# Kernel tuning notes

Measured on AMD Instinct MI355X. Metric: run time of the kernel, lower is better.

The kernel has to match this reference:

```python
import jax, jax.numpy as jnp
import numpy as np

B, LC, LT, D = 32, 2048, 512, 256  # D = 2*hidden_dim (bidirectional LSTM output)


def setup_inputs() -> dict:
    key = jax.random.key(0)
    k1, k2 = jax.random.split(key)
    return {
        "context_hidden": jax.random.normal(k1, (B, LC, D), dtype=jnp.float32),
        "target_hidden": jax.random.normal(k2, (B, LT, D), dtype=jnp.float32),
    }


def reference(context_hidden, target_hidden):
    # Pairwise Euclidean distance via |c|^2 + |t|^2 - 2 c.t (replaces the
    # original Python double for-loop of per-pair torch.norm calls).
    c2 = jnp.sum(context_hidden * context_hidden, axis=-1, keepdims=True)      # [B,Lc,1]
    t2 = jnp.sum(target_hidden * target_hidden, axis=-1)[:, None, :]           # [B,1,Lt]
    ct = jnp.einsum('bcd,btd->bct', context_hidden, target_hidden)             # [B,Lc,Lt]
    dist = jnp.sqrt(jnp.maximum(c2 + t2 - 2.0 * ct, 0.0))
    weights = 1.0 / (1.0 + dist)  # G2CT: [B,Lc,Lt]
    # G2C_m = weights @ target ; G2T_m = weights^T @ context (as in forward)
    g2c_m = jnp.einsum('bct,btd->bcd', weights, target_hidden)                 # [B,Lc,D]
    g2t_m = jnp.einsum('bct,bcd->btd', weights, context_hidden)                # [B,Lt,D]
    # concat along sequence axis so the block has a single output tensor
    return jnp.concatenate([g2c_m, g2t_m], axis=1)                             # [B,Lc+Lt,D]
```

## Files before the change

kernel.cpp:

```cpp
#include <hip/hip_runtime.h>

typedef float f32x4 __attribute__((ext_vector_type(4)));
typedef short s16x8 __attribute__((ext_vector_type(8)));

#define NB_    32
#define NLC    2048
#define NLT    512
#define ND     256
#define NCHUNK 512
#define NITER  (NCHUNK / 32)

__device__ __forceinline__ unsigned short f2bf(float f) {
    union { float f; unsigned int u; } v; v.f = f;
    unsigned int r = v.u + 0x7FFFu + ((v.u >> 16) & 1u);
    return (unsigned short)(r >> 16);
}

__device__ __forceinline__ s16x8 cvt8(float4 a, float4 c, float s) {
    s16x8 f;
    f[0]=(short)f2bf(s*a.x); f[1]=(short)f2bf(s*a.y); f[2]=(short)f2bf(s*a.z); f[3]=(short)f2bf(s*a.w);
    f[4]=(short)f2bf(s*c.x); f[5]=(short)f2bf(s*c.y); f[6]=(short)f2bf(s*c.z); f[7]=(short)f2bf(s*c.w);
    return f;
}

__device__ __forceinline__ void glds16(const void* g, void* l) {
    __builtin_amdgcn_global_load_lds(
        (const __attribute__((address_space(1))) unsigned int*)g,
        (__attribute__((address_space(3))) unsigned int*)l, 16, 0, 0);
}

__global__ __launch_bounds__(256) void prep_kernel(
    const float* __restrict__ ctx, const float* __restrict__ tgt,
    float* __restrict__ norms,
    unsigned short* __restrict__ ctxb, unsigned short* __restrict__ tgtb)
{
    const int wave = threadIdx.x >> 6;
    const int lane = threadIdx.x & 63;
    const int rid = blockIdx.x * 4 + wave;
    const float* row;
    unsigned short* drow;
    if (rid < NB_ * NLC) { row = ctx + (size_t)rid * ND; drow = ctxb + (size_t)rid * ND; }
    else { row = tgt + (size_t)(rid - NB_ * NLC) * ND; drow = tgtb + (size_t)(rid - NB_ * NLC) * ND; }
    const float4 v = *(const float4*)(row + lane * 4);
    *(ushort4*)(drow + lane * 4) = make_ushort4(f2bf(v.x), f2bf(v.y), f2bf(v.z), f2bf(v.w));
    float s = v.x * v.x + v.y * v.y + v.z * v.z + v.w * v.w;
    #pragma unroll
    for (int off = 32; off >= 1; off >>= 1) s += __shfl_xor(s, off);
    if (lane == 0) norms[rid] = s;
}

__global__ __launch_bounds__(256) void transpose_bf(
    const unsigned short* __restrict__ ctxb, const unsigned short* __restrict__ tgtb,
    unsigned short* __restrict__ ctxT, unsigned short* __restrict__ tgtT)
{
    __shared__ unsigned short tile[64][72];
    const int id = blockIdx.x;
    const unsigned short* in;
    unsigned short* outp;
    int ldL;
    if (id < 4096) {
        const int b = id >> 7, r = id & 127, lt = r >> 2, dt = r & 3;
        in   = ctxb + ((size_t)b * NLC + lt * 64) * ND + dt * 64;
        outp = ctxT + ((size_t)b * ND + dt * 64) * NLC + lt * 64;
        ldL = NLC;
    } else {
        const int id2 = id - 4096;
        const int b = id2 >> 5, r = id2 & 31, lt = r >> 2, dt = r & 3;
        in   = tgtb + ((size_t)b * NLT + lt * 64) * ND + dt * 64;
        outp = tgtT + ((size_t)b * ND + dt * 64) * NLT + lt * 64;
        ldL = NLT;
    }
    const int t = threadIdx.x;
    const int r0 = t >> 2, c0 = t & 3;
    const s16x8 v0 = *(const s16x8*)&in[(size_t)r0 * ND + c0 * 8];
    const s16x8 v1 = *(const s16x8*)&in[(size_t)r0 * ND + (c0 + 4) * 8];
    *(s16x8*)&tile[r0][c0 * 8] = v0;
    *(s16x8*)&tile[r0][(c0 + 4) * 8] = v1;
    __syncthreads();
    unsigned short buf[16];
    #pragma unroll
    for (int i = 0; i < 16; ++i) buf[i] = tile[(t & 3) * 16 + i][t >> 2];
    unsigned short* op = outp + (size_t)(t >> 2) * ldL + (t & 3) * 16;
    *(s16x8*)&op[0] = *(const s16x8*)&buf[0];
    *(s16x8*)&op[8] = *(const s16x8*)&buf[8];
}

__global__ __launch_bounds__(256, 2) void k1_weights(
    const unsigned short* __restrict__ ctxb, const unsigned short* __restrict__ tgtb,
    const float* __restrict__ norms,
    unsigned short* __restrict__ Wg, unsigned short* __restrict__ WTg)
{
    __shared__ __align__(16) unsigned short Alds[2][128 * 64];
    __shared__ __align__(16) unsigned short Blds[2][128 * 64];
    __shared__ __align__(16) unsigned short relay[4][16 * 128];

    const int phys = blockIdx.x;
    const int L = (phys & 7) * 256 + (phys >> 3);
    const int b = L >> 6;
    const int r = L & 63;
    const int cb = r >> 2, tb = r & 3;

    const int tid = threadIdx.x, wave = tid >> 6, lane = tid & 63;
    const int lr = lane & 15, lq = lane >> 4;
    const int cw = cb * 128 + wave * 32;

    const unsigned short* Actx = ctxb + ((size_t)b * NLC + cb * 128) * ND;
    const unsigned short* Btgt = tgtb + ((size_t)b * NLT + tb * 128) * ND;

    auto STAGE = [&](int buf, int ks) {
        #pragma unroll
        for (int i = 0; i < 4; ++i) {
            const int q = wave * 4 + i;
            const int rloc = q * 8 + (lane >> 3);
            const int gcol = (lane & 7) ^ (rloc & 7);
            glds16(Actx + (size_t)rloc * ND + ks * 64 + gcol * 8, &Alds[buf][q * 512]);
            glds16(Btgt + (size_t)rloc * ND + ks * 64 + gcol * 8, &Blds[buf][q * 512]);
        }
    };

    f32x4 acc[2][8];
    #pragma unroll
    for (int mf = 0; mf < 2; ++mf)
        #pragma unroll
        for (int nf = 0; nf < 8; ++nf) acc[mf][nf] = (f32x4)(0.0f);

    STAGE(0, 0);
    int buf = 0;
    for (int ks = 0; ks < 4; ++ks) {
        __syncthreads();
        if (ks < 3) STAGE(buf ^ 1, ks + 1);
        #pragma unroll
        for (int kk = 0; kk < 2; ++kk) {
            s16x8 af[2];
            #pragma unroll
            for (int mf = 0; mf < 2; ++mf) {
                const int row = wave * 32 + mf * 16 + lr;
                af[mf] = *(const s16x8*)&Alds[buf][row * 64 + (((kk * 4 + lq) ^ (row & 7)) * 8)];
            }
            #pragma unroll
            for (int nf = 0; nf < 8; ++nf) {
                const int row = nf * 16 + lr;
                const s16x8 bf = *(const s16x8*)&Blds[buf][row * 64 + (((kk * 4 + lq) ^ (row & 7)) * 8)];
                acc[0][nf] = __builtin_amdgcn_mfma_f32_16x16x32_bf16(af[0], bf, acc[0][nf], 0, 0, 0);
                acc[1][nf] = __builtin_amdgcn_mfma_f32_16x16x32_bf16(af[1], bf, acc[1][nf], 0, 0, 0);
            }
        }
        buf ^= 1;
    }

    float c2[2][4], t2[8];
    #pragma unroll
    for (int mf = 0; mf < 2; ++mf)
        #pragma unroll
        for (int j = 0; j < 4; ++j)
            c2[mf][j] = norms[b * NLC + cw + mf * 16 + lq * 4 + j];
    #pragma unroll
    for (int nf = 0; nf < 8; ++nf)
        t2[nf] = norms[NB_ * NLC + b * NLT + tb * 128 + nf * 16 + lr];

    __syncthreads();
    #pragma unroll
    for (int mf = 0; mf < 2; ++mf) {
        #pragma unroll
        for (int nf = 0; nf < 8; ++nf) {
            #pragma unroll
            for (int j = 0; j < 4; ++j) {
                float d2 = c2[mf][j] + t2[nf] - 2.0f * acc[mf][nf][j];
                d2 = d2 > 0.0f ? d2 : 0.0f;
                const float w = __builtin_amdgcn_rcpf(1.0f + __builtin_amdgcn_sqrtf(d2));
                const int row = lq * 4 + j;
                relay[wave][row * 128 + ((nf * 16 + lr) ^ ((row & 7) << 3))] = f2bf(w);
            }
        }
        __syncthreads();
        {
            const int rrow = lane >> 2;
            const int cbs = (lane & 3) * 32;
            const size_t wrow = ((size_t)b * NLC + cw + mf * 16 + rrow) * NLT + tb * 128;
            #pragma unroll
            for (int e = 0; e < 4; ++e) {
                const int colb = cbs + e * 8;
                const s16x8 v = *(const s16x8*)&relay[wave][rrow * 128 + (colb ^ ((rrow & 7) << 3))];
                *(s16x8*)&Wg[wrow + colb] = v;
            }
        }
        #pragma unroll
        for (int c = 0; c < 2; ++c) {
            const int tc = (lane << 1) | c;
            unsigned short colv[16];
            #pragma unroll
            for (int rr = 0; rr < 16; ++rr)
                colv[rr] = relay[wave][rr * 128 + (tc ^ ((rr & 7) << 3))];
            const size_t wtrow = ((size_t)b * NLT + tb * 128 + tc) * NLC + cw + mf * 16;
            *(s16x8*)&WTg[wtrow]     = *(const s16x8*)&colv[0];
            *(s16x8*)&WTg[wtrow + 8] = *(const s16x8*)&colv[8];
        }
        __syncthreads();
    }
}

__global__ __launch_bounds__(256, 2) void k23v2(
    const unsigned short* __restrict__ At, const unsigned short* __restrict__ Bw,
    float* __restrict__ outp, int mode)
{
    __shared__ __align__(16) unsigned short Slds[2][256 * 64];

    const int phys = blockIdx.x;
    const int L = (phys & 7) * 64 + (phys >> 3);
    int ldk;
    const unsigned short *Ab, *Bb;
    float* outB;
    if (mode == 2) {
        const int b = L >> 4, cb = L & 15;
        ldk = NLT;
        Ab = At + (size_t)b * ND * NLT;
        Bb = Bw + ((size_t)b * NLC + cb * 128) * NLT;
        outB = outp + ((size_t)b * (NLC + NLT) + cb * 128) * ND;
    } else {
        const int b = L >> 4, j = L & 15, cb = j & 3, ch = j >> 2;
        ldk = NLC;
        Ab = At + (size_t)b * ND * NLC + ch * 512;
        Bb = Bw + ((size_t)b * NLT + cb * 128) * NLC + ch * 512;
        outB = outp + ((size_t)(ch * NB_ + b) * NLT + cb * 128) * ND;
    }

    const int tid = threadIdx.x, wave = tid >> 6, lane = tid & 63;
    const int lr = lane & 15, lq = lane >> 4;

    const int srow = tid >> 3;
    const int schunk = tid & 7;

    auto STAGE = [&](int buf, int ks) {
        #pragma unroll
        for (int i = 0; i < 8; ++i) {
            const int row = i * 32 + srow;
            const int gcol = schunk ^ (row & 7);
            glds16(Ab + (size_t)row * ldk + ks * 64 + gcol * 8,
                   &Slds[buf][(i * 32 + wave * 8) * 64]);
        }
    };

    f32x4 acc[16][2];
    #pragma unroll
    for (int mf = 0; mf < 16; ++mf) { acc[mf][0] = (f32x4)(0.0f); acc[mf][1] = (f32x4)(0.0f); }

    STAGE(0, 0);
    for (int ks = 0; ks < 8; ++ks) {
        __syncthreads();
        const int buf = ks & 1;
        if (ks < 7) STAGE(buf ^ 1, ks + 1);

        s16x8 bfr[2][2];
        #pragma unroll
        for (int j = 0; j < 2; ++j)
            #pragma unroll
            for (int kk = 0; kk < 2; ++kk)
                bfr[j][kk] = *(const s16x8*)&Bb[(size_t)(wave * 32 + j * 16 + lr) * ldk +
                                                ks * 64 + kk * 32 + lq * 8];

        __builtin_amdgcn_s_setprio(1);
        #pragma unroll
        for (int kk = 0; kk < 2; ++kk) {
            #pragma unroll
            for (int mf = 0; mf < 16; ++mf) {
                const int row = mf * 16 + lr;
                const s16x8 af = *(const s16x8*)&Slds[buf][row * 64 +
                                                           (((kk * 4 + lq) ^ (row & 7)) * 8)];
                acc[mf][0] = __builtin_amdgcn_mfma_f32_16x16x32_bf16(af, bfr[0][kk], acc[mf][0], 0, 0, 0);
                acc[mf][1] = __builtin_amdgcn_mfma_f32_16x16x32_bf16(af, bfr[1][kk], acc[mf][1], 0, 0, 0);
            }
        }
        __builtin_amdgcn_s_setprio(0);
    }

    #pragma unroll
    for (int j = 0; j < 2; ++j) {
        const int col = wave * 32 + j * 16 + lr;
        float* rp = outB + (size_t)col * ND;
        #pragma unroll
        for (int mf = 0; mf < 16; ++mf) {
            const f32x4 v = acc[mf][j];
            *(float4*)(rp + mf * 16 + lq * 4) = make_float4(v[0], v[1], v[2], v[3]);
        }
    }
}

__global__ __launch_bounds__(256) void reduce_part(const float* __restrict__ part,
                                                   float* __restrict__ out) {
    const int g = blockIdx.x * 256 + threadIdx.x;
    #pragma unroll
    for (int k = 0; k < 4; ++k) {
        const int i = g + k * 262144;
        const int b = i >> 15;
        const int rem = i & 32767;
        const int t = rem >> 6;
        const int d4 = (rem & 63) * 4;
        const size_t base = ((size_t)b * NLT + t) * ND + d4;
        const float4 s0 = *(const float4*)(part + base);
        const float4 s1 = *(const float4*)(part + base + 4194304);
        const float4 s2 = *(const float4*)(part + base + 8388608);
        const float4 s3 = *(const float4*)(part + base + 12582912);
        *(float4*)(out + ((size_t)b * (NLC + NLT) + NLC + t) * ND + d4) =
            make_float4(s0.x + s1.x + s2.x + s3.x, s0.y + s1.y + s2.y + s3.y,
                        s0.z + s1.z + s2.z + s3.z, s0.w + s1.w + s2.w + s3.w);
    }
}

__global__ __launch_bounds__(256) void zero_g2t(float* __restrict__ out) {
    const int g = blockIdx.x * 256 + threadIdx.x;
    #pragma unroll
    for (int k = 0; k < 4; ++k) {
        const int i = g + k * 262144;
        const int bb = i >> 15;
        const int off = i & 32767;
        *(float4*)(out + ((size_t)bb * (NLC + NLT) + NLC) * ND + (size_t)off * 4) =
            make_float4(0.f, 0.f, 0.f, 0.f);
    }
}

__global__ __launch_bounds__(256) void reduce_g2t(const float* __restrict__ part,
                                                  float* __restrict__ out) {
    const int g = blockIdx.x * 256 + threadIdx.x;
    #pragma unroll
    for (int k = 0; k < 4; ++k) {
        const int i = g + k * 262144;
        const int b = i >> 15;
        const int rem = i & 32767;
        const int row = rem >> 6;
        const int d4 = (rem & 63) * 4;
        const int mb = row >> 7, r = row & 127;
        const size_t base = ((size_t)(b * 16 + mb * 4) * 32768) + (size_t)r * 256 + d4;
        float4 s0 = *(const float4*)(part + base);
        float4 s1 = *(const float4*)(part + base + 32768);
        float4 s2 = *(const float4*)(part + base + 65536);
        float4 s3 = *(const float4*)(part + base + 98304);
        *(float4*)(out + ((size_t)b * (NLC + NLT) + NLC + row) * ND + d4) =
            make_float4(s0.x + s1.x + s2.x + s3.x, s0.y + s1.y + s2.y + s3.y,
                        s0.z + s1.z + s2.z + s3.z, s0.w + s1.w + s2.w + s3.w);
    }
}

__global__ __launch_bounds__(256, 2) void fused_dist_attn(
    const float* __restrict__ ctx, const float* __restrict__ tgt,
    float* __restrict__ out, float* __restrict__ part)
{
    __shared__ __align__(16) unsigned short Klds[2][32 * 256];
    __shared__ __align__(16) unsigned short VTlds[2][256 * 32];
    __shared__ __align__(16) unsigned short Wlds[4 * 32 * 32];
    __shared__ unsigned int KextLds[2][32];

    const int phys = blockIdx.x;
    const int L = (phys & 7) * 128 + (phys >> 3);
    const int isB = (L & 1) == 0;
    const int idx = L >> 1;
    const int b = idx >> 4;
    const float *Q, *KV;
    size_t outbase;
    if (isB) {
        const int mb = (idx >> 2) & 3, nc = idx & 3;
        Q = tgt + ((size_t)b * NLT + mb * 128) * ND;
        KV = ctx + ((size_t)b * NLC + nc * NCHUNK) * ND;
        outbase = ((size_t)b * (NLC + NLT) + NLC + mb * 128) * ND;
    } else {
        const int mb = idx & 15;
        Q = ctx + ((size_t)b * NLC + mb * 128) * ND;
        KV = tgt + (size_t)b * NLT * ND;
        outbase = ((size_t)b * (NLC + NLT) + mb * 128) * ND;
    }

    const int tid = threadIdx.x, wave = tid >> 6, lane = tid & 63;
    const int lr = lane & 15, lq = lane >> 4;

    s16x8 qf[2][8];
    s16x8 qe[2];
    #pragma unroll
    for (int mf = 0; mf < 2; ++mf) {
        const float* qrow = Q + (size_t)(wave * 32 + mf * 16 + lr) * ND;
        float q2 = 0.0f;
        #pragma unroll
        for (int kk = 0; kk < 8; ++kk) {
            const float4 a = *(const float4*)(qrow + kk * 32 + lq * 8);
            const float4 c = *(const float4*)(qrow + kk * 32 + lq * 8 + 4);
            q2 += a.x*a.x + a.y*a.y + a.z*a.z + a.w*a.w;
            q2 += c.x*c.x + c.y*c.y + c.z*c.z + c.w*c.w;
            qf[mf][kk] = cvt8(a, c, -2.0f);
        }
        q2 += __shfl_xor(q2, 16);
        q2 += __shfl_xor(q2, 32);
        union { unsigned int u[4]; s16x8 v; } qu;
        qu.u[0] = (lq == 0) ? (0x3F80u | ((unsigned int)f2bf(q2) << 16)) : 0u;
        qu.u[1] = 0u; qu.u[2] = 0u; qu.u[3] = 0u;
        qe[mf] = qu.v;
    }

    f32x4 acc[2][16];
    #pragma unroll
    for (int mf = 0; mf < 2; ++mf)
        #pragma unroll
        for (int dt = 0; dt < 16; ++dt)
            acc[mf][dt] = (f32x4)(0.0f);

    const int r4 = 8 * wave + 4 * (lane & 1);
    const int d8 = (lane >> 1) * 8;
    float4 ldr[4][2];

    auto LOADT = [&](int n0) {
        #pragma unroll
        for (int rr = 0; rr < 4; ++rr)
            #pragma unroll
            for (int h = 0; h < 2; ++h)
                ldr[rr][h] = *(const float4*)(KV + (size_t)(n0 + r4 + rr) * ND + d8 + 4 * h);
    };

    auto WRITET = [&](int sel) {
        float ps[4];
        unsigned short kb[4][8];
        #pragma unroll
        for (int rr = 0; rr < 4; ++rr) {
            const float4 a = ldr[rr][0], c = ldr[rr][1];
            ps[rr] = a.x*a.x + a.y*a.y + a.z*a.z + a.w*a.w
                   + c.x*c.x + c.y*c.y + c.z*c.z + c.w*c.w;
            kb[rr][0]=f2bf(a.x); kb[rr][1]=f2bf(a.y); kb[rr][2]=f2bf(a.z); kb[rr][3]=f2bf(a.w);
            kb[rr][4]=f2bf(c.x); kb[rr][5]=f2bf(c.y); kb[rr][6]=f2bf(c.z); kb[rr][7]=f2bf(c.w);
            const int r = r4 + rr;
            *(s16x8*)&Klds[sel][r * 256 + (d8 ^ ((r & 7) << 3))] = *(const s16x8*)kb[rr];
        }
        #pragma unroll
        for (int dd = 0; dd < 8; ++dd) {
            const int d = d8 + dd;
            *(ushort4*)&VTlds[sel][d * 32 + (r4 ^ (((d >> 3) & 3) << 3))] =
                make_ushort4(kb[0][dd], kb[1][dd], kb[2][dd], kb[3][dd]);
        }
        #pragma unroll
        for (int rr = 0; rr < 4; ++rr) {
            ps[rr] += __shfl_xor(ps[rr], 2);
            ps[rr] += __shfl_xor(ps[rr], 4);
            ps[rr] += __shfl_xor(ps[rr], 8);
            ps[rr] += __shfl_xor(ps[rr], 16);
            ps[rr] += __shfl_xor(ps[rr], 32);
        }
        if (lane < 2) {
            #pragma unroll
            for (int rr = 0; rr < 4; ++rr)
                KextLds[sel][8 * wave + 4 * lane + rr] =
                    (unsigned int)f2bf(ps[rr]) | 0x3F800000u;
        }
    };

    LOADT(0);
    WRITET(0);

    #pragma unroll 2
    for (int t = 0; t < NITER; ++t) {
        __syncthreads();
        const int sel = t & 1;
        if (t + 1 < NITER) LOADT((t + 1) * 32);

        unsigned int p0 = 0u, p1 = 0u;
        if (lq == 0) { p0 = KextLds[sel][lr]; p1 = KextLds[sel][16 + lr]; }
        union { unsigned int u[4]; s16x8 v; } keu0, keu1;
        keu0.u[0] = p0; keu0.u[1] = 0; keu0.u[2] = 0; keu0.u[3] = 0;
        keu1.u[0] = p1; keu1.u[1] = 0; keu1.u[2] = 0; keu1.u[3] = 0;

        f32x4 sacc[2][2];
        sacc[0][0] = (f32x4)(0.0f); sacc[0][1] = (f32x4)(0.0f);
        sacc[1][0] = (f32x4)(0.0f); sacc[1][1] = (f32x4)(0.0f);
        __builtin_amdgcn_s_setprio(1);
        #pragma unroll
        for (int kk = 0; kk < 8; ++kk) {
            const int cs = (kk * 32 + lq * 8) ^ ((lr & 7) << 3);
            const s16x8 kf0 = *(const s16x8*)&Klds[sel][lr * 256 + cs];
            const s16x8 kf1 = *(const s16x8*)&Klds[sel][(16 + lr) * 256 + cs];
            sacc[0][0] = __builtin_amdgcn_mfma_f32_16x16x32_bf16(kf0, qf[0][kk], sacc[0][0], 0, 0, 0);
            sacc[0][1] = __builtin_amdgcn_mfma_f32_16x16x32_bf16(kf0, qf[1][kk], sacc[0][1], 0, 0, 0);
            sacc[1][0] = __builtin_amdgcn_mfma_f32_16x16x32_bf16(kf1, qf[0][kk], sacc[1][0], 0, 0, 0);
            sacc[1][1] = __builtin_amdgcn_mfma_f32_16x16x32_bf16(kf1, qf[1][kk], sacc[1][1], 0, 0, 0);
        }
        sacc[0][0] = __builtin_amdgcn_mfma_f32_16x16x32_bf16(keu0.v, qe[0], sacc[0][0], 0, 0, 0);
        sacc[0][1] = __builtin_amdgcn_mfma_f32_16x16x32_bf16(keu0.v, qe[1], sacc[0][1], 0, 0, 0);
        sacc[1][0] = __builtin_amdgcn_mfma_f32_16x16x32_bf16(keu1.v, qe[0], sacc[1][0], 0, 0, 0);
        sacc[1][1] = __builtin_amdgcn_mfma_f32_16x16x32_bf16(keu1.v, qe[1], sacc[1][1], 0, 0, 0);
        __builtin_amdgcn_s_setprio(0);

        #pragma unroll
        for (int ns = 0; ns < 2; ++ns) {
            #pragma unroll
            for (int mf = 0; mf < 2; ++mf) {
                unsigned short w4[4];
                #pragma unroll
                for (int j = 0; j < 4; ++j) {
                    float d2 = sacc[ns][mf][j];
                    d2 = d2 > 0.0f ? d2 : 0.0f;
                    w4[j] = f2bf(__builtin_amdgcn_rcpf(1.0f + __builtin_amdgcn_sqrtf(d2)));
                }
                const int row = mf * 16 + lr;
                const int col = (ns * 16 + lq * 4) ^ ((row & 3) << 3);
                *(ushort4*)&Wlds[wave * 1024 + row * 32 + col] =
                    make_ushort4(w4[0], w4[1], w4[2], w4[3]);
            }
        }

        s16x8 wfr[2];
        #pragma unroll
        for (int mf = 0; mf < 2; ++mf)
            wfr[mf] = *(const s16x8*)&Wlds[wave * 1024 + (mf * 16 + lr) * 32 +
                                           ((lq * 8) ^ ((lr & 3) << 3))];
        __builtin_amdgcn_s_setprio(1);
        #pragma unroll
        for (int dt = 0; dt < 16; ++dt) {
            const int vr = dt * 16 + lr;
            const s16x8 vf = *(const s16x8*)&VTlds[sel][vr * 32 +
                                                        ((lq * 8) ^ (((vr >> 3) & 3) << 3))];
            acc[0][dt] = __builtin_amdgcn_mfma_f32_16x16x32_bf16(vf, wfr[0], acc[0][dt], 0, 0, 0);
            acc[1][dt] = __builtin_amdgcn_mfma_f32_16x16x32_bf16(vf, wfr[1], acc[1][dt], 0, 0, 0);
        }
        __builtin_amdgcn_s_setprio(0);

        if (t + 1 < NITER) WRITET(sel ^ 1);
    }

    if (isB) {
        if (part) {
            float* p = part + (size_t)idx * 32768;
            #pragma unroll
            for (int mf = 0; mf < 2; ++mf) {
                const size_t rowbase = (size_t)(wave * 32 + mf * 16 + lr) * ND;
                #pragma unroll
                for (int dt = 0; dt < 16; ++dt) {
                    const f32x4 v = acc[mf][dt];
                    *(float4*)(p + rowbase + dt * 16 + lq * 4) = make_float4(v[0], v[1], v[2], v[3]);
                }
            }
        } else {
            #pragma unroll
            for (int mf = 0; mf < 2; ++mf) {
                float* rowp = out + outbase + (size_t)(wave * 32 + mf * 16 + lr) * ND;
                #pragma unroll
                for (int dt = 0; dt < 16; ++dt)
                    #pragma unroll
                    for (int j = 0; j < 4; ++j)
                        atomicAdd(rowp + dt * 16 + lq * 4 + j, acc[mf][dt][j]);
            }
        }
    } else {
        #pragma unroll
        for (int mf = 0; mf < 2; ++mf) {
            const size_t rowbase = outbase + (size_t)(wave * 32 + mf * 16 + lr) * ND;
            #pragma unroll
            for (int dt = 0; dt < 16; ++dt) {
                const f32x4 v = acc[mf][dt];
                *(float4*)(out + rowbase + dt * 16 + lq * 4) = make_float4(v[0], v[1], v[2], v[3]);
            }
        }
    }
}

extern "C" void kernel_launch(void* const* d_in, const int* in_sizes, int n_in,
                              void* d_out, int out_size, void* d_ws, size_t ws_size,
                              hipStream_t stream) {
    const float* ctx = (const float*)d_in[0];
    const float* tgt = (const float*)d_in[1];
    float* out = (float*)d_out;

    const size_t OFF_NORMS = 0;
    const size_t OFF_CTXB  = 327680;
    const size_t OFF_TGTB  = OFF_CTXB + 33554432;
    const size_t OFF_CTXT  = OFF_TGTB + 8388608;
    const size_t OFF_TGTT  = OFF_CTXT + 33554432;
    const size_t OFF_W     = OFF_TGTT + 8388608;
    const size_t OFF_WT    = OFF_W + 67108864;
    const size_t NEED_NEW  = OFF_WT + 67108864;

    char* ws = (char*)d_ws;
    if (ws_size >= NEED_NEW) {
        float* norms = (float*)(ws + OFF_NORMS);
        unsigned short* ctxb = (unsigned short*)(ws + OFF_CTXB);
        unsigned short* tgtb = (unsigned short*)(ws + OFF_TGTB);
        unsigned short* ctxT = (unsigned short*)(ws + OFF_CTXT);
        unsigned short* tgtT = (unsigned short*)(ws + OFF_TGTT);
        unsigned short* Wg   = (unsigned short*)(ws + OFF_W);
        unsigned short* WTg  = (unsigned short*)(ws + OFF_WT);
        float* part = (float*)(ws + OFF_W);

        prep_kernel<<<20480, 256, 0, stream>>>(ctx, tgt, norms, ctxb, tgtb);
        transpose_bf<<<5120, 256, 0, stream>>>(ctxb, tgtb, ctxT, tgtT);
        k1_weights<<<2048, 256, 0, stream>>>(ctxb, tgtb, norms, Wg, WTg);
        k23v2<<<512, 256, 0, stream>>>(tgtT, Wg, out, 2);
        k23v2<<<512, 256, 0, stream>>>(ctxT, WTg, part, 3);
        reduce_part<<<1024, 256, 0, stream>>>(part, out);
    } else {
        const size_t need = (size_t)512 * 128 * 256 * 4;
        if (ws_size >= need) {
            float* part = (float*)d_ws;
            fused_dist_attn<<<1024, 256, 0, stream>>>(ctx, tgt, out, part);
            reduce_g2t<<<1024, 256, 0, stream>>>(part, out);
        } else {
            zero_g2t<<<1024, 256, 0, stream>>>(out);
            fused_dist_attn<<<1024, 256, 0, stream>>>(ctx, tgt, out, nullptr);
        }
    }
}
```

Measured before the change: 188.9 us.

## Fuse weight computation with G2C matmul and drop split-K partial reduction

Result: slower. 330.1 us (+74.8%).

```diff
diff --git a/kernel.cpp b/kernel.cpp
--- a/kernel.cpp
+++ b/kernel.cpp
@@ -85,50 +85,78 @@
     *(s16x8*)&op[8] = *(const s16x8*)&buf[8];
 }
 
-__global__ __launch_bounds__(256, 2) void k1_weights(
+__global__ __launch_bounds__(256, 2) void k1f(
     const unsigned short* __restrict__ ctxb, const unsigned short* __restrict__ tgtb,
-    const float* __restrict__ norms,
-    unsigned short* __restrict__ Wg, unsigned short* __restrict__ WTg)
+    const unsigned short* __restrict__ tgtT, const float* __restrict__ norms,
+    unsigned short* __restrict__ WTg, float* __restrict__ out)
 {
     __shared__ __align__(16) unsigned short Alds[2][128 * 64];
-    __shared__ __align__(16) unsigned short Blds[2][128 * 64];
-    __shared__ __align__(16) unsigned short relay[4][16 * 128];
+    __shared__ __align__(16) unsigned short Blds[2][64 * 64];
+    __shared__ __align__(16) unsigned short relay[128 * 64];
 
     const int phys = blockIdx.x;
-    const int L = (phys & 7) * 256 + (phys >> 3);
-    const int b = L >> 6;
-    const int r = L & 63;
-    const int cb = r >> 2, tb = r & 3;
+    const int L = (phys & 7) * 64 + (phys >> 3);
+    const int b = L >> 4, cb = L & 15;
 
     const int tid = threadIdx.x, wave = tid >> 6, lane = tid & 63;
     const int lr = lane & 15, lq = lane >> 4;
-    const int cw = cb * 128 + wave * 32;
 
     const unsigned short* Actx = ctxb + ((size_t)b * NLC + cb * 128) * ND;
-    const unsigned short* Btgt = tgtb + ((size_t)b * NLT + tb * 128) * ND;
-
-    auto STAGE = [&](int buf, int ks) {
+    const unsigned short* Btgt = tgtb + (size_t)b * NLT * ND;
+    const unsigned short* Ttgt = tgtT + (size_t)b * ND * NLT;
+
+    auto STAGE_A = [&](int buf, int ks) {
         #pragma unroll
         for (int i = 0; i < 4; ++i) {
             const int q = wave * 4 + i;
             const int rloc = q * 8 + (lane >> 3);
             const int gcol = (lane & 7) ^ (rloc & 7);
             glds16(Actx + (size_t)rloc * ND + ks * 64 + gcol * 8, &Alds[buf][q * 512]);
-            glds16(Btgt + (size_t)rloc * ND + ks * 64 + gcol * 8, &Blds[buf][q * 512]);
         }
     };
-
-    f32x4 acc[2][8];
+    auto STAGE_B = [&](int buf, int tb, int ks) {
+        #pragma unroll
+        for (int i = 0; i < 2; ++i) {
+            const int q = wave * 2 + i;
+            const int rloc = q * 8 + (lane >> 3);
+            const int gcol = (lane & 7) ^ (rloc & 7);
+            glds16(Btgt + (size_t)(tb * 64 + rloc) * ND + ks * 64 + gcol * 8,
+                   &Blds[buf][q * 512]);
+        }
+    };
+
+    float c2[2][4];
     #pragma unroll
     for (int mf = 0; mf < 2; ++mf)
         #pragma unroll
-        for (int nf = 0; nf < 8; ++nf) acc[mf][nf] = (f32x4)(0.0f);
-
-    STAGE(0, 0);
-    int buf = 0;
-    for (int ks = 0; ks < 4; ++ks) {
+        for (int j = 0; j < 4; ++j)
+            c2[mf][j] = norms[b * NLC + cb * 128 + wave * 32 + mf * 16 + lq * 4 + j];
+
+    f32x4 pacc[4][8];
+    #pragma unroll
+    for (int mf = 0; mf < 4; ++mf)
+        #pragma unroll
+        for (int nf = 0; nf < 8; ++nf) pacc[mf][nf] = (f32x4)(0.0f);
+
+    STAGE_A(0, 0);
+    STAGE_B(0, 0, 0);
+
+    f32x4 sacc[2][4];
+    for (int step = 0; step < 32; ++step) {
+        const int tb = step >> 2, ks = step & 3;
+        const int buf = step & 1;
         __syncthreads();
-        if (ks < 3) STAGE(buf ^ 1, ks + 1);
+        if (step < 31) {
+            STAGE_A(buf ^ 1, (step + 1) & 3);
+            STAGE_B(buf ^ 1, (step + 1) >> 2, (step + 1) & 3);
+        }
+        if (ks == 0) {
+            #pragma unroll
+            for (int mf = 0; mf < 2; ++mf)
+                #pragma unroll
+                for (int nf = 0; nf < 4; ++nf) sacc[mf][nf] = (f32x4)(0.0f);
+        }
+        __builtin_amdgcn_s_setprio(1);
         #pragma unroll
         for (int kk = 0; kk < 2; ++kk) {
             s16x8 af[2];
@@ -138,171 +166,145 @@
                 af[mf] = *(const s16x8*)&Alds[buf][row * 64 + (((kk * 4 + lq) ^ (row & 7)) * 8)];
             }
             #pragma unroll
-            for (int nf = 0; nf < 8; ++nf) {
+            for (int nf = 0; nf < 4; ++nf) {
                 const int row = nf * 16 + lr;
                 const s16x8 bf = *(const s16x8*)&Blds[buf][row * 64 + (((kk * 4 + lq) ^ (row & 7)) * 8)];
-                acc[0][nf] = __builtin_amdgcn_mfma_f32_16x16x32_bf16(af[0], bf, acc[0][nf], 0, 0, 0);
-                acc[1][nf] = __builtin_amdgcn_mfma_f32_16x16x32_bf16(af[1], bf, acc[1][nf], 0, 0, 0);
-            }
-        }
-        buf ^= 1;
-    }
-
-    float c2[2][4], t2[8];
-    #pragma unroll
-    for (int mf = 0; mf < 2; ++mf)
-        #pragma unroll
-        for (int j = 0; j < 4; ++j)
-            c2[mf][j] = norms[b * NLC + cw + mf * 16 + lq * 4 + j];
-    #pragma unroll
-    for (int nf = 0; nf < 8; ++nf)
-        t2[nf] = norms[NB_ * NLC + b * NLT + tb * 128 + nf * 16 + lr];
-
-    __syncthreads();
-    #pragma unroll
-    for (int mf = 0; mf < 2; ++mf) {
-        #pragma unroll
-        for (int nf = 0; nf < 8; ++nf) {
-            #pragma unroll
-            for (int j = 0; j < 4; ++j) {
-                float d2 = c2[mf][j] + t2[nf] - 2.0f * acc[mf][nf][j];
-                d2 = d2 > 0.0f ? d2 : 0.0f;
-                const float w = __builtin_amdgcn_rcpf(1.0f + __builtin_amdgcn_sqrtf(d2));
-                const int row = lq * 4 + j;
-                relay[wave][row * 128 + ((nf * 16 + lr) ^ ((row & 7) << 3))] = f2bf(w);
-            }
-        }
-        __syncthreads();
-        {
-            const int rrow = lane >> 2;
-            const int cbs = (lane & 3) * 32;
-            const size_t wrow = ((size_t)b * NLC + cw + mf * 16 + rrow) * NLT + tb * 128;
-            #pragma unroll
-            for (int e = 0; e < 4; ++e) {
-                const int colb = cbs + e * 8;
-                const s16x8 v = *(const s16x8*)&relay[wave][rrow * 128 + (colb ^ ((rrow & 7) << 3))];
-                *(s16x8*)&Wg[wrow + colb] = v;
-            }
-        }
-        #pragma unroll
-        for (int c = 0; c < 2; ++c) {
-            const int tc = (lane << 1) | c;
-            unsigned short colv[16];
-            #pragma unroll
-            for (int rr = 0; rr < 16; ++rr)
-                colv[rr] = relay[wave][rr * 128 + (tc ^ ((rr & 7) << 3))];
-            const size_t wtrow = ((size_t)b * NLT + tb * 128 + tc) * NLC + cw + mf * 16;
-            *(s16x8*)&WTg[wtrow]     = *(const s16x8*)&colv[0];
-            *(s16x8*)&WTg[wtrow + 8] = *(const s16x8*)&colv[8];
-        }
-        __syncthreads();
-    }
-}
-
-__global__ __launch_bounds__(256, 2) void k23v2(
-    const unsigned short* __restrict__ At, const unsigned short* __restrict__ Bw,
-    float* __restrict__ outp, int mode)
+                sacc[0][nf] = __builtin_amdgcn_mfma_f32_16x16x32_bf16(af[0], bf, sacc[0][nf], 0, 0, 0);
+                sacc[1][nf] = __builtin_amdgcn_mfma_f32_16x16x32_bf16(af[1], bf, sacc[1][nf], 0, 0, 0);
+            }
+        }
+        __builtin_amdgcn_s_setprio(0);
+
+        if (ks == 3) {
+            #pragma unroll
+            for (int mf = 0; mf < 2; ++mf) {
+                #pragma unroll
+                for (int nf = 0; nf < 4; ++nf) {
+                    const float t2 = norms[NB_ * NLC + b * NLT + tb * 64 + nf * 16 + lr];
+                    #pragma unroll
+                    for (int j = 0; j < 4; ++j) {
+                        float d2 = c2[mf][j] + t2 - 2.0f * sacc[mf][nf][j];
+                        d2 = d2 > 0.0f ? d2 : 0.0f;
+                        const float w = __builtin_amdgcn_rcpf(1.0f + __builtin_amdgcn_sqrtf(d2));
+                        const int row = wave * 32 + mf * 16 + lq * 4 + j;
+                        relay[row * 64 + ((nf * 16 + lr) ^ ((row & 7) << 3))] = f2bf(w);
+                    }
+                }
+            }
+            __syncthreads();
+
+            {
+                const int trow = tid >> 2;
+                const int cchunk = (tid & 3) * 32;
+                const size_t wtrow = ((size_t)b * NLT + tb * 64 + trow) * NLC + cb * 128;
+                #pragma unroll
+                for (int e = 0; e < 4; ++e) {
+                    const int col8 = cchunk + e * 8;
+                    unsigned short v8[8];
+                    #pragma unroll
+                    for (int i = 0; i < 8; ++i) {
+                        const int c = col8 + i;
+                        v8[i] = relay[c * 64 + (trow ^ ((c & 7) << 3))];
+                    }
+                    *(s16x8*)&WTg[wtrow + col8] = *(const s16x8*)v8;
+                }
+            }
+
+            __builtin_amdgcn_s_setprio(1);
+            #pragma unroll
+            for (int kt = 0; kt < 2; ++kt) {
+                s16x8 bfr[8];
+                #pragma unroll
+                for (int nf = 0; nf < 8; ++nf) {
+                    const int c = nf * 16 + lr;
+                    bfr[nf] = *(const s16x8*)&relay[c * 64 + ((kt * 32 + lq * 8) ^ ((c & 7) << 3))];
+                }
+                #pragma unroll
+                for (int mf = 0; mf < 4; ++mf) {
+                    const int d = wave * 64 + mf * 16 + lr;
+                    const s16x8 af = *(const s16x8*)&Ttgt[(size_t)d * NLT + tb * 64 + kt * 32 + lq * 8];
+                    #pragma unroll
+                    for (int nf = 0; nf < 8; ++nf)
+                        pacc[mf][nf] = __builtin_amdgcn_mfma_f32_16x16x32_bf16(af, bfr[nf], pacc[mf][nf], 0, 0, 0);
+                }
+            }
+            __builtin_amdgcn_s_setprio(0);
+        }
+    }
+
+    #pragma unroll
+    for (int nf = 0; nf < 8; ++nf) {
+        float* rp = out + ((size_t)b * (NLC + NLT) + cb * 128 + nf * 16 + lr) * ND;
+        #pragma unroll
+        for (int mf = 0; mf < 4; ++mf) {
+            const f32x4 v = pacc[mf][nf];
+            *(float4*)(rp + wave * 64 + mf * 16 + lq * 4) = make_float4(v[0], v[1], v[2], v[3]);
+        }
+    }
+}
+
+__global__ __launch_bounds__(256, 2) void k3v3(
+    const unsigned short* __restrict__ ctxT, const unsigned short* __restrict__ WTg,
+    float* __restrict__ out)
 {
-    __shared__ __align__(16) unsigned short Slds[2][256 * 64];
+    __shared__ __align__(16) unsigned short Slds[2][64 * 64];
 
     const int phys = blockIdx.x;
     const int L = (phys & 7) * 64 + (phys >> 3);
-    int ldk;
-    const unsigned short *Ab, *Bb;
-    float* outB;
-    if (mode == 2) {
-        const int b = L >> 4, cb = L & 15;
-        ldk = NLT;
-        Ab = At + (size_t)b * ND * NLT;
-        Bb = Bw + ((size_t)b * NLC + cb * 128) * NLT;
-        outB = outp + ((size_t)b * (NLC + NLT) + cb * 128) * ND;
-    } else {
-        const int b = L >> 4, j = L & 15, cb = j & 3, ch = j >> 2;
-        ldk = NLC;
-        Ab = At + (size_t)b * ND * NLC + ch * 512;
-        Bb = Bw + ((size_t)b * NLT + cb * 128) * NLC + ch * 512;
-        outB = outp + ((size_t)(ch * NB_ + b) * NLT + cb * 128) * ND;
-    }
+    const int b = L >> 4, r = L & 15;
+    const int tb4 = r >> 2, dh = r & 3;
 
     const int tid = threadIdx.x, wave = tid >> 6, lane = tid & 63;
     const int lr = lane & 15, lq = lane >> 4;
 
-    const int srow = tid >> 3;
-    const int schunk = tid & 7;
+    const unsigned short* Ab = ctxT + (size_t)b * ND * NLC + (size_t)(dh * 64) * NLC;
+    const unsigned short* Bb = WTg + ((size_t)b * NLT + tb4 * 128) * NLC;
 
     auto STAGE = [&](int buf, int ks) {
         #pragma unroll
-        for (int i = 0; i < 8; ++i) {
-            const int row = i * 32 + srow;
-            const int gcol = schunk ^ (row & 7);
-            glds16(Ab + (size_t)row * ldk + ks * 64 + gcol * 8,
-                   &Slds[buf][(i * 32 + wave * 8) * 64]);
+        for (int i = 0; i < 2; ++i) {
+            const int q = wave * 2 + i;
+            const int rloc = q * 8 + (lane >> 3);
+            const int gcol = (lane & 7) ^ (rloc & 7);
+            glds16(Ab + (size_t)rloc * NLC + ks * 64 + gcol * 8, &Slds[buf][q * 512]);
         }
     };
 
-    f32x4 acc[16][2];
-    #pragma unroll
-    for (int mf = 0; mf < 16; ++mf) { acc[mf][0] = (f32x4)(0.0f); acc[mf][1] = (f32x4)(0.0f); }
+    f32x4 acc[8];
+    #pragma unroll
+    for (int nf = 0; nf < 8; ++nf) acc[nf] = (f32x4)(0.0f);
 
     STAGE(0, 0);
-    for (int ks = 0; ks < 8; ++ks) {
+    for (int ks = 0; ks < 32; ++ks) {
         __syncthreads();
         const int buf = ks & 1;
-        if (ks < 7) STAGE(buf ^ 1, ks + 1);
-
-        s16x8 bfr[2][2];
-        #pragma unroll
-        for (int j = 0; j < 2; ++j)
+        if (ks < 31) STAGE(buf ^ 1, ks + 1);
+
+        s16x8 bfr[8][2];
+        #pragma unroll
+        for (int nf = 0; nf < 8; ++nf)
             #pragma unroll
             for (int kk = 0; kk < 2; ++kk)
-                bfr[j][kk] = *(const s16x8*)&Bb[(size_t)(wave * 32 + j * 16 + lr) * ldk +
-                                                ks * 64 + kk * 32 + lq * 8];
-
+                bfr[nf][kk] = *(const s16x8*)&Bb[(size_t)(nf * 16 + lr) * NLC +
+                                                 ks * 64 + kk * 32 + lq * 8];
         __builtin_amdgcn_s_setprio(1);
         #pragma unroll
         for (int kk = 0; kk < 2; ++kk) {
-            #pragma unroll
-            for (int mf = 0; mf < 16; ++mf) {
-                const int row = mf * 16 + lr;
-                const s16x8 af = *(const s16x8*)&Slds[buf][row * 64 +
-                                                           (((kk * 4 + lq) ^ (row & 7)) * 8)];
-                acc[mf][0] = __builtin_amdgcn_mfma_f32_16x16x32_bf16(af, bfr[0][kk], acc[mf][0], 0, 0, 0);
-                acc[mf][1] = __builtin_amdgcn_mfma_f32_16x16x32_bf16(af, bfr[1][kk], acc[mf][1], 0, 0, 0);
-            }
+            const int row = wave * 16 + lr;
+            const s16x8 af = *(const s16x8*)&Slds[buf][row * 64 + (((kk * 4 + lq) ^ (row & 7)) * 8)];
+            #pragma unroll
+            for (int nf = 0; nf < 8; ++nf)
+                acc[nf] = __builtin_amdgcn_mfma_f32_16x16x32_bf16(af, bfr[nf][kk], acc[nf], 0, 0, 0);
         }
         __builtin_amdgcn_s_setprio(0);
     }
 
     #pragma unroll
-    for (int j = 0; j < 2; ++j) {
-        const int col = wave * 32 + j * 16 + lr;
-        float* rp = outB + (size_t)col * ND;
-        #pragma unroll
-        for (int mf = 0; mf < 16; ++mf) {
-            const f32x4 v = acc[mf][j];
-            *(float4*)(rp + mf * 16 + lq * 4) = make_float4(v[0], v[1], v[2], v[3]);
-        }
-    }
-}
-
-__global__ __launch_bounds__(256) void reduce_part(const float* __restrict__ part,
-                                                   float* __restrict__ out) {
-    const int g = blockIdx.x * 256 + threadIdx.x;
-    #pragma unroll
-    for (int k = 0; k < 4; ++k) {
-        const int i = g + k * 262144;
-        const int b = i >> 15;
-        const int rem = i & 32767;
-        const int t = rem >> 6;
-        const int d4 = (rem & 63) * 4;
-        const size_t base = ((size_t)b * NLT + t) * ND + d4;
-        const float4 s0 = *(const float4*)(part + base);
-        const float4 s1 = *(const float4*)(part + base + 4194304);
-        const float4 s2 = *(const float4*)(part + base + 8388608);
-        const float4 s3 = *(const float4*)(part + base + 12582912);
-        *(float4*)(out + ((size_t)b * (NLC + NLT) + NLC + t) * ND + d4) =
-            make_float4(s0.x + s1.x + s2.x + s3.x, s0.y + s1.y + s2.y + s3.y,
-                        s0.z + s1.z + s2.z + s3.z, s0.w + s1.w + s2.w + s3.w);
+    for (int nf = 0; nf < 8; ++nf) {
+        const int t = tb4 * 128 + nf * 16 + lr;
+        const f32x4 v = acc[nf];
+        *(float4*)(out + ((size_t)b * (NLC + NLT) + NLC + t) * ND + dh * 64 + wave * 16 + lq * 4) =
+            make_float4(v[0], v[1], v[2], v[3]);
     }
 }
 
@@ -328,8 +330,8 @@
         const int rem = i & 32767;
         const int row = rem >> 6;
         const int d4 = (rem & 63) * 4;
-        const int mb = row >> 7, r = row & 127;
-        const size_t base = ((size_t)(b * 16 + mb * 4) * 32768) + (size_t)r * 256 + d4;
+        const int mb = row >> 7, rr = row & 127;
+        const size_t base = ((size_t)(b * 16 + mb * 4) * 32768) + (size_t)rr * 256 + d4;
         float4 s0 = *(const float4*)(part + base);
         float4 s1 = *(const float4*)(part + base + 32768);
         float4 s2 = *(const float4*)(part + base + 65536);
@@ -567,8 +569,7 @@
     const size_t OFF_TGTB  = OFF_CTXB + 33554432;
     const size_t OFF_CTXT  = OFF_TGTB + 8388608;
     const size_t OFF_TGTT  = OFF_CTXT + 33554432;
-    const size_t OFF_W     = OFF_TGTT + 8388608;
-    const size_t OFF_WT    = OFF_W + 67108864;
+    const size_t OFF_WT    = OFF_TGTT + 8388608;
     const size_t NEED_NEW  = OFF_WT + 67108864;
 
     char* ws = (char*)d_ws;
@@ -578,16 +579,12 @@
         unsigned short* tgtb = (unsigned short*)(ws + OFF_TGTB);
         unsigned short* ctxT = (unsigned short*)(ws + OFF_CTXT);
         unsigned short* tgtT = (unsigned short*)(ws + OFF_TGTT);
-        unsigned short* Wg   = (unsigned short*)(ws + OFF_W);
         unsigned short* WTg  = (unsigned short*)(ws + OFF_WT);
-        float* part = (float*)(ws + OFF_W);
 
         prep_kernel<<<20480, 256, 0, stream>>>(ctx, tgt, norms, ctxb, tgtb);
         transpose_bf<<<5120, 256, 0, stream>>>(ctxb, tgtb, ctxT, tgtT);
-        k1_weights<<<2048, 256, 0, stream>>>(ctxb, tgtb, norms, Wg, WTg);
-        k23v2<<<512, 256, 0, stream>>>(tgtT, Wg, out, 2);
-        k23v2<<<512, 256, 0, stream>>>(ctxT, WTg, part, 3);
-        reduce_part<<<1024, 256, 0, stream>>>(part, out);
+        k1f<<<512, 256, 0, stream>>>(ctxb, tgtb, tgtT, norms, WTg, out);
+        k3v3<<<512, 256, 0, stream>>>(ctxT, WTg, out);
     } else {
         const size_t need = (size_t)512 * 128 * 256 * 4;
         if (ws_size >= need) {
```

## Drop split-K for G2T GEMM and stage transposed weights through LDS

Applied to the files above, without the earlier changes.

New measurement: 257.9 us. +36.5%, slower.

```diff
diff --git a/kernel.cpp b/kernel.cpp
--- a/kernel.cpp
+++ b/kernel.cpp
@@ -159,18 +159,24 @@
         t2[nf] = norms[NB_ * NLC + b * NLT + tb * 128 + nf * 16 + lr];
 
     __syncthreads();
+    unsigned short* WTs = (unsigned short*)Alds;
+
     #pragma unroll
     for (int mf = 0; mf < 2; ++mf) {
         #pragma unroll
         for (int nf = 0; nf < 8; ++nf) {
+            unsigned short w4[4];
             #pragma unroll
             for (int j = 0; j < 4; ++j) {
                 float d2 = c2[mf][j] + t2[nf] - 2.0f * acc[mf][nf][j];
                 d2 = d2 > 0.0f ? d2 : 0.0f;
-                const float w = __builtin_amdgcn_rcpf(1.0f + __builtin_amdgcn_sqrtf(d2));
+                w4[j] = f2bf(__builtin_amdgcn_rcpf(1.0f + __builtin_amdgcn_sqrtf(d2)));
                 const int row = lq * 4 + j;
-                relay[wave][row * 128 + ((nf * 16 + lr) ^ ((row & 7) << 3))] = f2bf(w);
-            }
+                relay[wave][row * 128 + ((nf * 16 + lr) ^ ((row & 7) << 3))] = w4[j];
+            }
+            const int t = nf * 16 + lr;
+            const int c4 = (wave * 32 + mf * 16 + lq * 4) ^ ((t & 15) << 3);
+            *(ushort4*)&WTs[t * 128 + c4] = make_ushort4(w4[0], w4[1], w4[2], w4[3]);
         }
         __syncthreads();
         {
@@ -184,45 +190,33 @@
                 *(s16x8*)&Wg[wrow + colb] = v;
             }
         }
-        #pragma unroll
-        for (int c = 0; c < 2; ++c) {
-            const int tc = (lane << 1) | c;
-            unsigned short colv[16];
-            #pragma unroll
-            for (int rr = 0; rr < 16; ++rr)
-                colv[rr] = relay[wave][rr * 128 + (tc ^ ((rr & 7) << 3))];
-            const size_t wtrow = ((size_t)b * NLT + tb * 128 + tc) * NLC + cw + mf * 16;
-            *(s16x8*)&WTg[wtrow]     = *(const s16x8*)&colv[0];
-            *(s16x8*)&WTg[wtrow + 8] = *(const s16x8*)&colv[8];
-        }
         __syncthreads();
     }
-}
-
-__global__ __launch_bounds__(256, 2) void k23v2(
+
+    {
+        const int trow = tid >> 1;
+        const int cseg = (tid & 1) * 64;
+        const size_t wtrow = ((size_t)b * NLT + tb * 128 + trow) * NLC + cb * 128 + cseg;
+        #pragma unroll
+        for (int e = 0; e < 8; ++e) {
+            const int c8 = (cseg + e * 8) ^ ((trow & 15) << 3);
+            *(s16x8*)&WTg[wtrow + e * 8] = *(const s16x8*)&WTs[trow * 128 + c8];
+        }
+    }
+}
+
+__global__ __launch_bounds__(256, 2) void k2_gemm(
     const unsigned short* __restrict__ At, const unsigned short* __restrict__ Bw,
-    float* __restrict__ outp, int mode)
+    float* __restrict__ outp)
 {
     __shared__ __align__(16) unsigned short Slds[2][256 * 64];
 
     const int phys = blockIdx.x;
     const int L = (phys & 7) * 64 + (phys >> 3);
-    int ldk;
-    const unsigned short *Ab, *Bb;
-    float* outB;
-    if (mode == 2) {
-        const int b = L >> 4, cb = L & 15;
-        ldk = NLT;
-        Ab = At + (size_t)b * ND * NLT;
-        Bb = Bw + ((size_t)b * NLC + cb * 128) * NLT;
-        outB = outp + ((size_t)b * (NLC + NLT) + cb * 128) * ND;
-    } else {
-        const int b = L >> 4, j = L & 15, cb = j & 3, ch = j >> 2;
-        ldk = NLC;
-        Ab = At + (size_t)b * ND * NLC + ch * 512;
-        Bb = Bw + ((size_t)b * NLT + cb * 128) * NLC + ch * 512;
-        outB = outp + ((size_t)(ch * NB_ + b) * NLT + cb * 128) * ND;
-    }
+    const int b = L >> 4, cb = L & 15;
+    const unsigned short* Ab = At + (size_t)b * ND * NLT;
+    const unsigned short* Bb = Bw + ((size_t)b * NLC + cb * 128) * NLT;
+    float* outB = outp + ((size_t)b * (NLC + NLT) + cb * 128) * ND;
 
     const int tid = threadIdx.x, wave = tid >> 6, lane = tid & 63;
     const int lr = lane & 15, lq = lane >> 4;
@@ -235,7 +229,7 @@
         for (int i = 0; i < 8; ++i) {
             const int row = i * 32 + srow;
             const int gcol = schunk ^ (row & 7);
-            glds16(Ab + (size_t)row * ldk + ks * 64 + gcol * 8,
+            glds16(Ab + (size_t)row * NLT + ks * 64 + gcol * 8,
                    &Slds[buf][(i * 32 + wave * 8) * 64]);
         }
     };
@@ -255,7 +249,7 @@
         for (int j = 0; j < 2; ++j)
             #pragma unroll
             for (int kk = 0; kk < 2; ++kk)
-                bfr[j][kk] = *(const s16x8*)&Bb[(size_t)(wave * 32 + j * 16 + lr) * ldk +
+                bfr[j][kk] = *(const s16x8*)&Bb[(size_t)(wave * 32 + j * 16 + lr) * NLT +
                                                 ks * 64 + kk * 32 + lq * 8];
 
         __builtin_amdgcn_s_setprio(1);
@@ -285,24 +279,68 @@
     }
 }
 
-__global__ __launch_bounds__(256) void reduce_part(const float* __restrict__ part,
-                                                   float* __restrict__ out) {
-    const int g = blockIdx.x * 256 + threadIdx.x;
-    #pragma unroll
-    for (int k = 0; k < 4; ++k) {
-        const int i = g + k * 262144;
-        const int b = i >> 15;
-        const int rem = i & 32767;
-        const int t = rem >> 6;
-        const int d4 = (rem & 63) * 4;
-        const size_t base = ((size_t)b * NLT + t) * ND + d4;
-        const float4 s0 = *(const float4*)(part + base);
-        const float4 s1 = *(const float4*)(part + base + 4194304);
-        const float4 s2 = *(const float4*)(part + base + 8388608);
-        const float4 s3 = *(const float4*)(part + base + 12582912);
-        *(float4*)(out + ((size_t)b * (NLC + NLT) + NLC + t) * ND + d4) =
-            make_float4(s0.x + s1.x + s2.x + s3.x, s0.y + s1.y + s2.y + s3.y,
-                        s0.z + s1.z + s2.z + s3.z, s0.w + s1.w + s2.w + s3.w);
+__global__ __launch_bounds__(256, 2) void k3v3(
+    const unsigned short* __restrict__ ctxT, const unsigned short* __restrict__ WTg,
+    float* __restrict__ out)
+{
+    __shared__ __align__(16) unsigned short Slds[2][64 * 64];
+
+    const int phys = blockIdx.x;
+    const int L = (phys & 7) * 64 + (phys >> 3);
+    const int b = L >> 4, r = L & 15;
+    const int tb4 = r >> 2, dh = r & 3;
+
+    const int tid = threadIdx.x, wave = tid >> 6, lane = tid & 63;
+    const int lr = lane & 15, lq = lane >> 4;
+
+    const unsigned short* Ab = ctxT + (size_t)b * ND * NLC + (size_t)(dh * 64) * NLC;
+    const unsigned short* Bb = WTg + ((size_t)b * NLT + tb4 * 128) * NLC;
+
+    auto STAGE = [&](int buf, int ks) {
+        #pragma unroll
+        for (int i = 0; i < 2; ++i) {
+            const int q = wave * 2 + i;
+            const int rloc = q * 8 + (lane >> 3);
+            const int gcol = (lane & 7) ^ (rloc & 7);
+            glds16(Ab + (size_t)rloc * NLC + ks * 64 + gcol * 8, &Slds[buf][q * 512]);
+        }
+    };
+
+    f32x4 acc[8];
+    #pragma unroll
+    for (int nf = 0; nf < 8; ++nf) acc[nf] = (f32x4)(0.0f);
+
+    STAGE(0, 0);
+    for (int ks = 0; ks < 32; ++ks) {
+        __syncthreads();
+        const int buf = ks & 1;
+        if (ks < 31) STAGE(buf ^ 1, ks + 1);
+
+        s16x8 bfr[8][2];
+        #pragma unroll
+        for (int nf = 0; nf < 8; ++nf)
+            #pragma unroll
+            for (int kk = 0; kk < 2; ++kk)
+                bfr[nf][kk] = *(const s16x8*)&Bb[(size_t)(nf * 16 + lr) * NLC +
+                                                 ks * 64 + kk * 32 + lq * 8];
+        __builtin_amdgcn_s_setprio(1);
+        #pragma unroll
+        for (int kk = 0; kk < 2; ++kk) {
+            const int row = wave * 16 + lr;
+            const s16x8 af = *(const s16x8*)&Slds[buf][row * 64 + (((kk * 4 + lq) ^ (row & 7)) * 8)];
+            #pragma unroll
+            for (int nf = 0; nf < 8; ++nf)
+                acc[nf] = __builtin_amdgcn_mfma_f32_16x16x32_bf16(af, bfr[nf][kk], acc[nf], 0, 0, 0);
+        }
+        __builtin_amdgcn_s_setprio(0);
+    }
+
+    #pragma unroll
+    for (int nf = 0; nf < 8; ++nf) {
+        const int t = tb4 * 128 + nf * 16 + lr;
+        const f32x4 v = acc[nf];
+        *(float4*)(out + ((size_t)b * (NLC + NLT) + NLC + t) * ND + dh * 64 + wave * 16 + lq * 4) =
+            make_float4(v[0], v[1], v[2], v[3]);
     }
 }
 
@@ -328,8 +366,8 @@
         const int rem = i & 32767;
         const int row = rem >> 6;
         const int d4 = (rem & 63) * 4;
-        const int mb = row >> 7, r = row & 127;
-        const size_t base = ((size_t)(b * 16 + mb * 4) * 32768) + (size_t)r * 256 + d4;
+        const int mb = row >> 7, rr = row & 127;
+        const size_t base = ((size_t)(b * 16 + mb * 4) * 32768) + (size_t)rr * 256 + d4;
         float4 s0 = *(const float4*)(part + base);
         float4 s1 = *(const float4*)(part + base + 32768);
         float4 s2 = *(const float4*)(part + base + 65536);
@@ -580,14 +618,12 @@
         unsigned short* tgtT = (unsigned short*)(ws + OFF_TGTT);
         unsigned short* Wg   = (unsigned short*)(ws + OFF_W);
         unsigned short* WTg  = (unsigned short*)(ws + OFF_WT);
-        float* part = (float*)(ws + OFF_W);
 
         prep_kernel<<<20480, 256, 0, stream>>>(ctx, tgt, norms, ctxb, tgtb);
         transpose_bf<<<5120, 256, 0, stream>>>(ctxb, tgtb, ctxT, tgtT);
         k1_weights<<<2048, 256, 0, stream>>>(ctxb, tgtb, norms, Wg, WTg);
-        k23v2<<<512, 256, 0, stream>>>(tgtT, Wg, out, 2);
-        k23v2<<<512, 256, 0, stream>>>(ctxT, WTg, part, 3);
-        reduce_part<<<1024, 256, 0, stream>>>(part, out);
+        k2_gemm<<<512, 256, 0, stream>>>(tgtT, Wg, out);
+        k3v3<<<512, 256, 0, stream>>>(ctxT, WTg, out);
     } else {
         const size_t need = (size_t)512 * 128 * 256 * 4;
         if (ws_size >= need) {
```
